# Kernel tuning notes

Hardware: AMD Instinct MI355X
Metric: run time of the kernel (lower is better)

The kernel has to match this reference:

```python
import jax, jax.numpy as jnp
import numpy as np

H = 4096  # hidden_size == input_size


def setup_inputs() -> dict:
    key = jax.random.key(0)
    ks = jax.random.split(key, 12)
    s = 0.02  # weight init scale
    return {
        "x": jax.random.normal(ks[0], (H,), jnp.float32),
        "h_prev": jnp.zeros((H,), jnp.float32),
        "C_prev": jax.random.normal(ks[1], (H, H), jnp.float32) * 0.01,
        "n_prev": jax.random.uniform(ks[2], (H,), jnp.float32) + 1.0,
        # projection weights (hidden_size x input_size) and biases
        "Wq": jax.random.normal(ks[3], (H, H), jnp.float32) * s,
        "Wk": jax.random.normal(ks[4], (H, H), jnp.float32) * s,
        "Wv": jax.random.normal(ks[5], (H, H), jnp.float32) * s,
        "Wo": jax.random.normal(ks[6], (H, H), jnp.float32) * s,
        "bq": jnp.zeros((H,), jnp.float32),
        "bk": jnp.zeros((H,), jnp.float32),
        "bv": jnp.zeros((H,), jnp.float32),
        "bo": jnp.zeros((H,), jnp.float32),
        # scalar input/forget gates: w^T x + b
        "wi": jax.random.normal(ks[7], (H,), jnp.float32) * s,
        "bi": jnp.zeros((), jnp.float32),
        "wf": jax.random.normal(ks[8], (H,), jnp.float32) * s,
        "bf": jnp.ones((), jnp.float32),  # bias forget gate toward remembering
    }


def reference(x, h_prev, C_prev, n_prev, Wq, Wk, Wv, Wo,
              bq, bk, bv, bo, wi, bi, wf, bf):
    # mLSTM single-step cell (xLSTM matrix memory). h_prev is unused by the
    # mLSTM math (no hidden-to-hidden recurrence), matching the CUDA layer API.
    d = jnp.asarray(Wk.shape[0], x.dtype)
    q = Wq @ x + bq                                   # [H]
    k = (Wk @ x + bk) / jnp.sqrt(d)                   # [H], scaled key
    v = Wv @ x + bv                                   # [H]
    i_gate = jnp.exp(jnp.dot(wi, x) + bi)             # scalar exponential input gate
    f_gate = jax.nn.sigmoid(jnp.dot(wf, x) + bf)      # scalar sigmoid forget gate
    # covariance-style rank-1 matrix-memory update
    C = f_gate * C_prev + i_gate * jnp.outer(v, k)    # [H, H]
    n = f_gate * n_prev + i_gate * k                  # [H]
    # normalized readout
    denom = jnp.maximum(jnp.abs(jnp.dot(n, q)), jnp.asarray(1.0, x.dtype))
    h_tilde = (C @ q) / denom                         # [H]
    o_gate = jax.nn.sigmoid(Wo @ x + bo)              # [H] output gate
    h = o_gate * h_tilde
    return (h, C, n)
```

## Files before the change

### kernel.cpp

```cpp
#include <hip/hip_runtime.h>
#include <math.h>

#define H 4096
#define HWORDS4 (H / 4)
#define ITERS (HWORDS4 / 64)

__device__ __forceinline__ float wave_reduce_sum(float v) {
    #pragma unroll
    for (int off = 32; off > 0; off >>= 1)
        v += __shfl_down(v, off, 64);
    return v;
}

__device__ __forceinline__ float sigmoidf_(float x) {
    return 1.0f / (1.0f + __expf(-x));
}

__global__ __launch_bounds__(256) void gemv_all(
    const float* __restrict__ x,
    const float* __restrict__ Wq, const float* __restrict__ Wk,
    const float* __restrict__ Wv, const float* __restrict__ Wo,
    const float* __restrict__ bq, const float* __restrict__ bk,
    const float* __restrict__ bv, const float* __restrict__ bo,
    const float* __restrict__ wi, const float* __restrict__ wf,
    float* __restrict__ q, float* __restrict__ k,
    float* __restrict__ v, float* __restrict__ og,
    float* __restrict__ s2)
{
    const int wave = threadIdx.x >> 6;
    const int lane = threadIdx.x & 63;
    const int rowId = blockIdx.x * 4 + wave;
    if (rowId >= 4 * H + 2) return;

    const int m = rowId >> 12;
    const int r = rowId & (H - 1);

    const float* row;
    if (rowId < 4 * H) {
        const float* W = (m == 0) ? Wq : (m == 1) ? Wk : (m == 2) ? Wv : Wo;
        row = W + (size_t)r * H;
    } else {
        row = (rowId == 4 * H) ? wi : wf;
    }

    const float4* row4 = (const float4*)row;
    const float4* x4   = (const float4*)x;

    float sum = 0.0f;
    #pragma unroll
    for (int it = 0; it < ITERS; ++it) {
        const int idx = it * 64 + lane;
        float4 a = row4[idx];
        float4 b = x4[idx];
        sum += a.x * b.x + a.y * b.y + a.z * b.z + a.w * b.w;
    }
    sum = wave_reduce_sum(sum);

    if (lane == 0) {
        if (rowId < 4 * H) {
            if (m == 0)      q[r]  = sum + bq[r];
            else if (m == 1) k[r]  = (sum + bk[r]) * 0.015625f;
            else if (m == 2) v[r]  = sum + bv[r];
            else             og[r] = sigmoidf_(sum + bo[r]);
        } else {
            s2[rowId - 4 * H] = sum;
        }
    }
}

__global__ __launch_bounds__(256) void c_update(
    const float* __restrict__ C_prev,
    const float* __restrict__ q, const float* __restrict__ k,
    const float* __restrict__ v, const float* __restrict__ s2,
    const float* __restrict__ bi, const float* __restrict__ bf,
    float* __restrict__ C_out, float* __restrict__ u)
{
    const int wave = threadIdx.x >> 6;
    const int lane = threadIdx.x & 63;
    const int r = blockIdx.x * 4 + wave;

    const float ig = __expf(s2[0] + bi[0]);
    const float fg = sigmoidf_(s2[1] + bf[0]);
    const float ivr = ig * v[r];

    const float4* c4 = (const float4*)(C_prev + (size_t)r * H);
    float4*       o4 = (float4*)(C_out + (size_t)r * H);
    const float4* q4 = (const float4*)q;
    const float4* k4 = (const float4*)k;

    float acc = 0.0f;
    #pragma unroll
    for (int it = 0; it < ITERS; ++it) {
        const int idx = it * 64 + lane;
        float4 c  = c4[idx];
        float4 qq = q4[idx];
        float4 kk = k4[idx];
        float4 o;
        o.x = fg * c.x + ivr * kk.x;
        o.y = fg * c.y + ivr * kk.y;
        o.z = fg * c.z + ivr * kk.z;
        o.w = fg * c.w + ivr * kk.w;
        o4[idx] = o;
        acc += c.x * qq.x + c.y * qq.y + c.z * qq.z + c.w * qq.w;
    }
    acc = wave_reduce_sum(acc);
    if (lane == 0) u[r] = acc;
}

__global__ __launch_bounds__(1024) void finalize(
    const float* __restrict__ n_prev,
    const float* __restrict__ q, const float* __restrict__ k,
    const float* __restrict__ v, const float* __restrict__ og,
    const float* __restrict__ u, const float* __restrict__ s2,
    const float* __restrict__ bi, const float* __restrict__ bf,
    float* __restrict__ h, float* __restrict__ n_out)
{
    const int t = threadIdx.x;
    const int wave = t >> 6;
    const int lane = t & 63;

    const float ig = __expf(s2[0] + bi[0]);
    const float fg = sigmoidf_(s2[1] + bf[0]);

    float nq = 0.0f, kq = 0.0f;
    for (int j = t; j < H; j += 1024) {
        float kj = k[j];
        float qj = q[j];
        float nj = fg * n_prev[j] + ig * kj;
        n_out[j] = nj;
        nq += nj * qj;
        kq += kj * qj;
    }
    nq = wave_reduce_sum(nq);
    kq = wave_reduce_sum(kq);

    __shared__ float snq[16], skq[16];
    if (lane == 0) { snq[wave] = nq; skq[wave] = kq; }
    __syncthreads();
    if (t == 0) {
        float a = 0.0f, b = 0.0f;
        #pragma unroll
        for (int w = 0; w < 16; ++w) { a += snq[w]; b += skq[w]; }
        snq[0] = a; skq[0] = b;
    }
    __syncthreads();

    const float denom = fmaxf(fabsf(snq[0]), 1.0f);
    const float kqv = skq[0];
    const float inv_denom = 1.0f / denom;

    for (int j = t; j < H; j += 1024) {
        float ht = (fg * u[j] + ig * v[j] * kqv) * inv_denom;
        h[j] = og[j] * ht;
    }
}

extern "C" void kernel_launch(void* const* d_in, const int* in_sizes, int n_in,
                              void* d_out, int out_size, void* d_ws, size_t ws_size,
                              hipStream_t stream) {
    const float* x      = (const float*)d_in[0];
    const float* C_prev = (const float*)d_in[2];
    const float* n_prev = (const float*)d_in[3];
    const float* Wq     = (const float*)d_in[4];
    const float* Wk     = (const float*)d_in[5];
    const float* Wv     = (const float*)d_in[6];
    const float* Wo     = (const float*)d_in[7];
    const float* bq     = (const float*)d_in[8];
    const float* bk     = (const float*)d_in[9];
    const float* bv     = (const float*)d_in[10];
    const float* bo     = (const float*)d_in[11];
    const float* wi     = (const float*)d_in[12];
    const float* bi     = (const float*)d_in[13];
    const float* wf     = (const float*)d_in[14];
    const float* bf     = (const float*)d_in[15];

    float* out   = (float*)d_out;
    float* h_out = out;
    float* C_out = out + H;
    float* n_out = out + H + (size_t)H * H;

    float* ws = (float*)d_ws;
    float* q  = ws;
    float* k  = ws + H;
    float* v  = ws + 2 * H;
    float* og = ws + 3 * H;
    float* u  = ws + 4 * H;
    float* s2 = ws + 5 * H;

    const int nrows = 4 * H + 2;
    const int blocks1 = (nrows + 3) / 4;
    gemv_all<<<blocks1, 256, 0, stream>>>(x, Wq, Wk, Wv, Wo, bq, bk, bv, bo,
                                          wi, wf, q, k, v, og, s2);

    c_update<<<H / 4, 256, 0, stream>>>(C_prev, q, k, v, s2, bi, bf, C_out, u);

    finalize<<<1, 1024, 0, stream>>>(n_prev, q, k, v, og, u, s2, bi, bf,
                                     h_out, n_out);
}
```

Baseline: 337.3 us.

## Stage x/q/k in LDS, multi-row blocks with batched loads, nontemporal C stores

The GEMV kernel now stages x in shared memory and has each block process 16 rows, loading a whole row segment into registers before the dot product. The gate dot products move to two dedicated blocks. The C update kernel stages q and k in LDS, handles 8 rows per block, batches its C_prev loads, and writes C_out with nontemporal stores to cut cache pollution. Finalize is vectorized to float4. The aim is more memory-level parallelism and fewer redundant global loads in this bandwidth-bound workload, at the cost of extra LDS traffic and register pressure.

```diff
diff --git a/kernel.cpp b/kernel.cpp
--- a/kernel.cpp
+++ b/kernel.cpp
@@ -2,8 +2,9 @@
 #include <math.h>
 
 #define H 4096
-#define HWORDS4 (H / 4)
-#define ITERS (HWORDS4 / 64)
+#define NB_GEMV 1024
+
+typedef float nfloat4 __attribute__((ext_vector_type(4)));
 
 __device__ __forceinline__ float wave_reduce_sum(float v) {
     #pragma unroll
@@ -16,7 +17,7 @@
     return 1.0f / (1.0f + __expf(-x));
 }
 
-__global__ __launch_bounds__(256) void gemv_all(
+__global__ __launch_bounds__(256, 4) void gemv_all(
     const float* __restrict__ x,
     const float* __restrict__ Wq, const float* __restrict__ Wk,
     const float* __restrict__ Wv, const float* __restrict__ Wo,
@@ -27,84 +28,113 @@
     float* __restrict__ v, float* __restrict__ og,
     float* __restrict__ s2)
 {
-    const int wave = threadIdx.x >> 6;
-    const int lane = threadIdx.x & 63;
-    const int rowId = blockIdx.x * 4 + wave;
-    if (rowId >= 4 * H + 2) return;
-
-    const int m = rowId >> 12;
-    const int r = rowId & (H - 1);
-
-    const float* row;
-    if (rowId < 4 * H) {
-        const float* W = (m == 0) ? Wq : (m == 1) ? Wk : (m == 2) ? Wv : Wo;
-        row = W + (size_t)r * H;
-    } else {
-        row = (rowId == 4 * H) ? wi : wf;
-    }
-
-    const float4* row4 = (const float4*)row;
-    const float4* x4   = (const float4*)x;
-
-    float sum = 0.0f;
+    __shared__ float4 xs[H / 4];
+    __shared__ float red[4];
+    const int t = threadIdx.x;
+    const float4* x4 = (const float4*)x;
+
+    if (blockIdx.x >= NB_GEMV) {
+        const float4* w4 = (const float4*)((blockIdx.x == NB_GEMV) ? wi : wf);
+        float s = 0.0f;
+        #pragma unroll
+        for (int i = 0; i < 4; ++i) {
+            float4 a = w4[i * 256 + t];
+            float4 b = x4[i * 256 + t];
+            s += a.x * b.x + a.y * b.y + a.z * b.z + a.w * b.w;
+        }
+        s = wave_reduce_sum(s);
+        const int wave = t >> 6, lane = t & 63;
+        if (lane == 0) red[wave] = s;
+        __syncthreads();
+        if (t == 0) s2[blockIdx.x - NB_GEMV] = red[0] + red[1] + red[2] + red[3];
+        return;
+    }
+
     #pragma unroll
-    for (int it = 0; it < ITERS; ++it) {
-        const int idx = it * 64 + lane;
-        float4 a = row4[idx];
-        float4 b = x4[idx];
-        sum += a.x * b.x + a.y * b.y + a.z * b.z + a.w * b.w;
-    }
-    sum = wave_reduce_sum(sum);
-
-    if (lane == 0) {
-        if (rowId < 4 * H) {
-            if (m == 0)      q[r]  = sum + bq[r];
-            else if (m == 1) k[r]  = (sum + bk[r]) * 0.015625f;
-            else if (m == 2) v[r]  = sum + bv[r];
-            else             og[r] = sigmoidf_(sum + bo[r]);
-        } else {
-            s2[rowId - 4 * H] = sum;
-        }
-    }
-}
-
-__global__ __launch_bounds__(256) void c_update(
+    for (int i = 0; i < 4; ++i) xs[i * 256 + t] = x4[i * 256 + t];
+    __syncthreads();
+
+    const int wave = t >> 6, lane = t & 63;
+    const int rowBase = blockIdx.x * 16;
+    const int m = rowBase >> 12;
+    const float* W = (m == 0) ? Wq : (m == 1) ? Wk : (m == 2) ? Wv : Wo;
+
+    #pragma unroll 1
+    for (int i = 0; i < 4; ++i) {
+        const int r = (rowBase & (H - 1)) + i * 4 + wave;
+        const float4* row4 = (const float4*)(W + (size_t)r * H);
+
+        float4 a[16];
+        #pragma unroll
+        for (int it = 0; it < 16; ++it) a[it] = row4[it * 64 + lane];
+
+        float acc = 0.0f;
+        #pragma unroll
+        for (int it = 0; it < 16; ++it) {
+            float4 b = xs[it * 64 + lane];
+            acc += a[it].x * b.x + a[it].y * b.y + a[it].z * b.z + a[it].w * b.w;
+        }
+        acc = wave_reduce_sum(acc);
+
+        if (lane == 0) {
+            if (m == 0)      q[r]  = acc + bq[r];
+            else if (m == 1) k[r]  = (acc + bk[r]) * 0.015625f;
+            else if (m == 2) v[r]  = acc + bv[r];
+            else             og[r] = sigmoidf_(acc + bo[r]);
+        }
+    }
+}
+
+__global__ __launch_bounds__(256, 2) void c_update(
     const float* __restrict__ C_prev,
     const float* __restrict__ q, const float* __restrict__ k,
     const float* __restrict__ v, const float* __restrict__ s2,
     const float* __restrict__ bi, const float* __restrict__ bf,
     float* __restrict__ C_out, float* __restrict__ u)
 {
-    const int wave = threadIdx.x >> 6;
-    const int lane = threadIdx.x & 63;
-    const int r = blockIdx.x * 4 + wave;
-
+    __shared__ float4 qs[H / 4];
+    __shared__ float4 ks[H / 4];
+    const int t = threadIdx.x;
+    const float4* q4 = (const float4*)q;
+    const float4* k4 = (const float4*)k;
+    #pragma unroll
+    for (int i = 0; i < 4; ++i) {
+        qs[i * 256 + t] = q4[i * 256 + t];
+        ks[i * 256 + t] = k4[i * 256 + t];
+    }
+    __syncthreads();
+
+    const int wave = t >> 6, lane = t & 63;
     const float ig = __expf(s2[0] + bi[0]);
     const float fg = sigmoidf_(s2[1] + bf[0]);
-    const float ivr = ig * v[r];
-
-    const float4* c4 = (const float4*)(C_prev + (size_t)r * H);
-    float4*       o4 = (float4*)(C_out + (size_t)r * H);
-    const float4* q4 = (const float4*)q;
-    const float4* k4 = (const float4*)k;
-
-    float acc = 0.0f;
-    #pragma unroll
-    for (int it = 0; it < ITERS; ++it) {
-        const int idx = it * 64 + lane;
-        float4 c  = c4[idx];
-        float4 qq = q4[idx];
-        float4 kk = k4[idx];
-        float4 o;
-        o.x = fg * c.x + ivr * kk.x;
-        o.y = fg * c.y + ivr * kk.y;
-        o.z = fg * c.z + ivr * kk.z;
-        o.w = fg * c.w + ivr * kk.w;
-        o4[idx] = o;
-        acc += c.x * qq.x + c.y * qq.y + c.z * qq.z + c.w * qq.w;
-    }
-    acc = wave_reduce_sum(acc);
-    if (lane == 0) u[r] = acc;
+
+    #pragma unroll 1
+    for (int i = 0; i < 2; ++i) {
+        const int r = blockIdx.x * 8 + i * 4 + wave;
+        const float4* c4 = (const float4*)(C_prev + (size_t)r * H);
+        nfloat4*      o4 = (nfloat4*)(C_out + (size_t)r * H);
+        const float ivr = ig * v[r];
+
+        float4 c[16];
+        #pragma unroll
+        for (int it = 0; it < 16; ++it) c[it] = c4[it * 64 + lane];
+
+        float acc = 0.0f;
+        #pragma unroll
+        for (int it = 0; it < 16; ++it) {
+            float4 qq = qs[it * 64 + lane];
+            float4 kk = ks[it * 64 + lane];
+            nfloat4 o;
+            o.x = fg * c[it].x + ivr * kk.x;
+            o.y = fg * c[it].y + ivr * kk.y;
+            o.z = fg * c[it].z + ivr * kk.z;
+            o.w = fg * c[it].w + ivr * kk.w;
+            __builtin_nontemporal_store(o, &o4[it * 64 + lane]);
+            acc += c[it].x * qq.x + c[it].y * qq.y + c[it].z * qq.z + c[it].w * qq.w;
+        }
+        acc = wave_reduce_sum(acc);
+        if (lane == 0) u[r] = acc;
+    }
 }
 
 __global__ __launch_bounds__(1024) void finalize(
@@ -122,15 +152,22 @@
     const float ig = __expf(s2[0] + bi[0]);
     const float fg = sigmoidf_(s2[1] + bf[0]);
 
-    float nq = 0.0f, kq = 0.0f;
-    for (int j = t; j < H; j += 1024) {
-        float kj = k[j];
-        float qj = q[j];
-        float nj = fg * n_prev[j] + ig * kj;
-        n_out[j] = nj;
-        nq += nj * qj;
-        kq += kj * qj;
-    }
+    const float4* q4  = (const float4*)q;
+    const float4* k4  = (const float4*)k;
+    const float4* np4 = (const float4*)n_prev;
+
+    float4 qq = q4[t];
+    float4 kk = k4[t];
+    float4 nn = np4[t];
+    float4 no;
+    no.x = fg * nn.x + ig * kk.x;
+    no.y = fg * nn.y + ig * kk.y;
+    no.z = fg * nn.z + ig * kk.z;
+    no.w = fg * nn.w + ig * kk.w;
+    ((float4*)n_out)[t] = no;
+
+    float nq = no.x * qq.x + no.y * qq.y + no.z * qq.z + no.w * qq.w;
+    float kq = kk.x * qq.x + kk.y * qq.y + kk.z * qq.z + kk.w * qq.w;
     nq = wave_reduce_sum(nq);
     kq = wave_reduce_sum(kq);
 
@@ -149,10 +186,18 @@
     const float kqv = skq[0];
     const float inv_denom = 1.0f / denom;
 
-    for (int j = t; j < H; j += 1024) {
-        float ht = (fg * u[j] + ig * v[j] * kqv) * inv_denom;
-        h[j] = og[j] * ht;
-    }
+    const float4* v4  = (const float4*)v;
+    const float4* og4 = (const float4*)og;
+    const float4* u4  = (const float4*)u;
+    float4 vv = v4[t];
+    float4 oo = og4[t];
+    float4 uu = u4[t];
+    float4 hh;
+    hh.x = oo.x * (fg * uu.x + ig * vv.x * kqv) * inv_denom;
+    hh.y = oo.y * (fg * uu.y + ig * vv.y * kqv) * inv_denom;
+    hh.z = oo.z * (fg * uu.z + ig * vv.z * kqv) * inv_denom;
+    hh.w = oo.w * (fg * uu.w + ig * vv.w * kqv) * inv_denom;
+    ((float4*)h)[t] = hh;
 }
 
 extern "C" void kernel_launch(void* const* d_in, const int* in_sizes, int n_in,
@@ -187,12 +232,10 @@
     float* u  = ws + 4 * H;
     float* s2 = ws + 5 * H;
 
-    const int nrows = 4 * H + 2;
-    const int blocks1 = (nrows + 3) / 4;
-    gemv_all<<<blocks1, 256, 0, stream>>>(x, Wq, Wk, Wv, Wo, bq, bk, bv, bo,
-                                          wi, wf, q, k, v, og, s2);
-
-    c_update<<<H / 4, 256, 0, stream>>>(C_prev, q, k, v, s2, bi, bf, C_out, u);
+    gemv_all<<<NB_GEMV + 2, 256, 0, stream>>>(x, Wq, Wk, Wv, Wo, bq, bk, bv, bo,
+                                              wi, wf, q, k, v, og, s2);
+
+    c_update<<<H / 8, 256, 0, stream>>>(C_prev, q, k, v, s2, bi, bf, C_out, u);
 
     finalize<<<1, 1024, 0, stream>>>(n_prev, q, k, v, og, u, s2, bi, bf,
                                      h_out, n_out);
```

New measurement: 338.2 us. No clear change (+0.3%).
